# Kernel optimization log

Hardware: AMD Instinct MI355X
Metric: run time of the kernel (lower is better)

Reference implementation:

```python
import jax, jax.numpy as jnp
import numpy as np

D_MODEL = 768
N_HEADS = 12
NUM_EXPERTS = 4
TOP_K = 2
SPAN_LEN = 64
GATE_HIDDEN = 128


def setup_inputs() -> dict:
    key = jax.random.key(0)
    ks = jax.random.split(key, 14)
    B, T, C, E = 4, 4096, D_MODEL, NUM_EXPERTS
    s = 0.02
    return {
        "hidden_states": jax.random.normal(ks[0], (B, T, C), jnp.float32),
        "Wq": jax.random.normal(ks[1], (E, C, C), jnp.float32) * s,
        "bq": jnp.zeros((E, C), jnp.float32),
        "Wk": jax.random.normal(ks[2], (E, C, C), jnp.float32) * s,
        "bk": jnp.zeros((E, C), jnp.float32),
        "Wv": jax.random.normal(ks[3], (E, C, C), jnp.float32) * s,
        "bv": jnp.zeros((E, C), jnp.float32),
        "gW1": jax.random.normal(ks[4], (GATE_HIDDEN, C), jnp.float32) * s,
        "gb1": jnp.zeros((GATE_HIDDEN,), jnp.float32),
        "gW2": jax.random.normal(ks[5], (E, GATE_HIDDEN), jnp.float32) * s,
        "gb2": jnp.zeros((E,), jnp.float32),
        "Wo": jax.random.normal(ks[6], (C, C), jnp.float32) * s,
        "bo": jnp.zeros((C,), jnp.float32),
    }


def _moe_proj(w, x, W, b):
    # per-expert projection then gate-weighted sum over experts
    # x: (B,N,S,C), W: (E,O,C), w: (B,N,E)
    proj = jnp.einsum("bnsc,eoc->ebnso", x, W)          # (E,B,N,S,C)
    out = jnp.einsum("bne,ebnso->bnso", w, proj)
    out = out + jnp.einsum("bne,eo->bno", w, b)[:, :, None, :]
    return out


def reference(hidden_states, Wq, bq, Wk, bk, Wv, bv, gW1, gb1, gW2, gb2, Wo, bo):
    B, T, C = hidden_states.shape
    S, H, E, K = SPAN_LEN, N_HEADS, NUM_EXPERTS, TOP_K
    Dh = C // H
    N = T // S  # T is a multiple of span_len -> no padding, all-ones masks
    x = hidden_states.reshape(B, N, S, C)

    # gating: mean-pool per span -> MLP -> top-k softmax scattered to E slots
    pooled = x.mean(axis=2)                                  # (B,N,C)
    h = jax.nn.relu(pooled @ gW1.T + gb1)
    logits = h @ gW2.T + gb2                                 # (B,N,E)
    vals, idx = jax.lax.top_k(logits, K)
    sm = jax.nn.softmax(vals, axis=-1)                       # (B,N,K)
    w = jnp.sum(jax.nn.one_hot(idx, E, dtype=sm.dtype) * sm[..., None], axis=-2)  # (B,N,E)
    entropy = -jnp.mean(jnp.sum(w * jnp.log(jnp.clip(w, 1e-9)), axis=-1))

    # gate-weighted expert QKV projections
    q = _moe_proj(w, x, Wq, bq).reshape(B, N, S, H, Dh)
    k = _moe_proj(w, x, Wk, bk).reshape(B, N, S, H, Dh)
    v = _moe_proj(w, x, Wv, bv).reshape(B, N, S, H, Dh)

    # per-span attention (mask is all ones; dropout in eval mode)
    scores = jnp.einsum("bnshd,bnthd->bnhst", q, k) / jnp.sqrt(jnp.float32(Dh))
    attn = jax.nn.softmax(scores, axis=-1)
    out = jnp.einsum("bnhst,bnthd->bnshd", attn, v).reshape(B, T, C)
    out = out @ Wo.T + bo
    return out, entropy
```

## Files before the change

### kernel.cpp

```cpp
#include <hip/hip_runtime.h>
#include <hip/hip_bf16.h>
#include <hip/hip_fp16.h>

typedef _Float16 f16;
typedef _Float16 f16x8 __attribute__((ext_vector_type(8)));
typedef _Float16 f16x4 __attribute__((ext_vector_type(4)));
typedef float f32x4 __attribute__((ext_vector_type(4)));

constexpr int B = 4;
constexpr int T = 4096;
constexpr int C = 768;
constexpr int NH = 12;
constexpr int DH = 64;
constexpr int E = 4;
constexpr int SPAN = 64;
constexpr int N = T / SPAN;
constexpr int BN = B * N;
constexpr int GH = 128;
constexpr int BTC = B * T * C;

constexpr int U_X  = BTC / 8;
constexpr int U_WE = E * C * C / 8;
constexpr int U_WO = C * C / 8;
constexpr int U_TOT = U_X + 3 * U_WE + U_WO;

__global__ void cvt_all(const float* __restrict__ x,
                        const float* __restrict__ Wq, const float* __restrict__ Wk,
                        const float* __restrict__ Wv, const float* __restrict__ Wo,
                        f16* __restrict__ x16,
                        f16* __restrict__ Wq16, f16* __restrict__ Wk16,
                        f16* __restrict__ Wv16, f16* __restrict__ Wo16) {
    int i = blockIdx.x * blockDim.x + threadIdx.x;
    int stride = gridDim.x * blockDim.x;
    for (; i < U_TOT; i += stride) {
        const float* src; f16* dst; int u;
        if (i < U_X)                { src = x;  dst = x16;  u = i; }
        else if (i < U_X + U_WE)    { src = Wq; dst = Wq16; u = i - U_X; }
        else if (i < U_X + 2*U_WE)  { src = Wk; dst = Wk16; u = i - U_X - U_WE; }
        else if (i < U_X + 3*U_WE)  { src = Wv; dst = Wv16; u = i - U_X - 2*U_WE; }
        else                        { src = Wo; dst = Wo16; u = i - U_X - 3*U_WE; }
        float4 a = ((const float4*)src)[2 * u];
        float4 b = ((const float4*)src)[2 * u + 1];
        f16x8 o;
        o[0] = (f16)a.x; o[1] = (f16)a.y; o[2] = (f16)a.z; o[3] = (f16)a.w;
        o[4] = (f16)b.x; o[5] = (f16)b.y; o[6] = (f16)b.z; o[7] = (f16)b.w;
        ((f16x8*)dst)[u] = o;
    }
}

__global__ void gate_kernel(const float* __restrict__ x,
                            const float* __restrict__ gW1, const float* __restrict__ gb1,
                            const float* __restrict__ gW2, const float* __restrict__ gb2,
                            int* __restrict__ eidx, float* __restrict__ ewts,
                            float* __restrict__ ent_partial) {
    int span = blockIdx.x;
    int tid = threadIdx.x;
    __shared__ float pooled[C];
    __shared__ float h[GH];
    __shared__ float logits[E];

    const float* xb = x + (size_t)span * SPAN * C;
    for (int c = tid; c < C; c += 256) {
        float s = 0.f;
        #pragma unroll 8
        for (int t = 0; t < SPAN; ++t) s += xb[t * C + c];
        pooled[c] = s * (1.f / 64.f);
    }
    __syncthreads();

    if (tid < GH) {
        float acc = gb1[tid];
        const float* wrow = gW1 + (size_t)tid * C;
        #pragma unroll 8
        for (int c = 0; c < C; ++c) acc += pooled[c] * wrow[c];
        h[tid] = acc > 0.f ? acc : 0.f;
    }
    __syncthreads();

    if (tid < E) {
        float acc = gb2[tid];
        const float* wrow = gW2 + (size_t)tid * GH;
        #pragma unroll 8
        for (int j = 0; j < GH; ++j) acc += h[j] * wrow[j];
        logits[tid] = acc;
    }
    __syncthreads();

    if (tid == 0) {
        int i0 = 0; float v0 = logits[0];
        for (int e = 1; e < E; ++e) { if (logits[e] > v0) { v0 = logits[e]; i0 = e; } }
        int i1 = -1; float v1 = -3.0e38f;
        for (int e = 0; e < E; ++e) { if (e != i0 && logits[e] > v1) { v1 = logits[e]; i1 = e; } }
        float bq_ = expf(v1 - v0);
        float s = 1.f + bq_;
        float sm0 = 1.f / s;
        float sm1 = bq_ / s;
        eidx[span * 2 + 0] = i0;
        eidx[span * 2 + 1] = i1;
        ewts[span * 2 + 0] = sm0;
        ewts[span * 2 + 1] = sm1;
        float p0 = fmaxf(sm0, 1e-9f), p1 = fmaxf(sm1, 1e-9f);
        ent_partial[span] = sm0 * logf(p0) + sm1 * logf(p1);
    }
}

__global__ void entropy_kernel(const float* __restrict__ ent_partial, float* __restrict__ out_ent) {
    __shared__ float sh[256];
    int tid = threadIdx.x;
    sh[tid] = ent_partial[tid];
    __syncthreads();
    for (int s = 128; s > 0; s >>= 1) {
        if (tid < s) sh[tid] += sh[tid + s];
        __syncthreads();
    }
    if (tid == 0) *out_ent = -sh[0] * (1.0f / (float)BN);
}

__global__ __launch_bounds__(256) void qkv_mfma(
    const f16* __restrict__ xh,
    const f16* __restrict__ Wq16, const float* __restrict__ bq,
    const f16* __restrict__ Wk16, const float* __restrict__ bk,
    const f16* __restrict__ Wv16, const float* __restrict__ bv,
    const int* __restrict__ eidx, const float* __restrict__ ewts,
    f16* __restrict__ q16, f16* __restrict__ k16, f16* __restrict__ vt)
{
    int span  = blockIdx.x;
    int otile = blockIdx.y;
    int proj  = blockIdx.z;

    const f16* W; const float* bias; f16* out;
    if (proj == 0)      { W = Wq16; bias = bq; out = q16; }
    else if (proj == 1) { W = Wk16; bias = bk; out = k16; }
    else                { W = Wv16; bias = bv; out = vt; }

    int e0 = eidx[span * 2 + 0], e1 = eidx[span * 2 + 1];
    float w0 = ewts[span * 2 + 0], w1 = ewts[span * 2 + 1];
    f16 w0h = (f16)w0, w1h = (f16)w1;

    __shared__ f16x8 xs_u[64 * 8];
    __shared__ f16x8 ws_u[256 * 8];

    const f16x8* xu  = (const f16x8*)(xh + (size_t)span * 64 * C);
    const f16x8* Wu0 = (const f16x8*)(W + ((size_t)e0 * C + otile * 256) * (size_t)C);
    const f16x8* Wu1 = (const f16x8*)(W + ((size_t)e1 * C + otile * 256) * (size_t)C);

    int tid = threadIdx.x;
    int lane = tid & 63, wv = tid >> 6;
    int lr = lane & 15, lg = lane >> 4;

    int xr0 = tid >> 3, xu0 = tid & 7;
    f32x4 acc[4][4] = {};

    f16x8 xr[2], w0r[8], w1r[8];
    #pragma unroll
    for (int i = 0; i < 2; ++i) {
        int id = tid + i * 256;
        xr[i] = xu[(id >> 3) * 96 + (id & 7)];
    }
    #pragma unroll
    for (int i = 0; i < 8; ++i) {
        int id = tid + i * 256;
        w0r[i] = Wu0[(size_t)(id >> 3) * 96 + (id & 7)];
        w1r[i] = Wu1[(size_t)(id >> 3) * 96 + (id & 7)];
    }

    for (int kc8 = 0; kc8 < 96; kc8 += 8) {
        #pragma unroll
        for (int i = 0; i < 2; ++i) {
            int id = tid + i * 256;
            int r = id >> 3, u = id & 7;
            xs_u[r * 8 + (u ^ (r & 7))] = xr[i];
        }
        #pragma unroll
        for (int i = 0; i < 8; ++i) {
            int id = tid + i * 256;
            int r = id >> 3, u = id & 7;
            ws_u[r * 8 + (u ^ (r & 7))] = w0r[i] * w0h + w1r[i] * w1h;
        }
        __syncthreads();

        if (kc8 < 88) {
            int kn = kc8 + 8;
            #pragma unroll
            for (int i = 0; i < 2; ++i) {
                int id = tid + i * 256;
                xr[i] = xu[(id >> 3) * 96 + kn + (id & 7)];
            }
            #pragma unroll
            for (int i = 0; i < 8; ++i) {
                int id = tid + i * 256;
                w0r[i] = Wu0[(size_t)(id >> 3) * 96 + kn + (id & 7)];
                w1r[i] = Wu1[(size_t)(id >> 3) * 96 + kn + (id & 7)];
            }
        }

        #pragma unroll
        for (int kk = 0; kk < 2; ++kk) {
            int ub = kk * 4 + lg;
            f16x8 afrag[4], bfrag[4];
            #pragma unroll
            for (int m = 0; m < 4; ++m) {
                int r = m * 16 + lr;
                afrag[m] = xs_u[r * 8 + (ub ^ (r & 7))];
            }
            #pragma unroll
            for (int n = 0; n < 4; ++n) {
                int r = wv * 64 + n * 16 + lr;
                bfrag[n] = ws_u[r * 8 + (ub ^ (r & 7))];
            }
            #pragma unroll
            for (int m = 0; m < 4; ++m)
                #pragma unroll
                for (int n = 0; n < 4; ++n)
                    acc[m][n] = __builtin_amdgcn_mfma_f32_16x16x32_f16(afrag[m], bfrag[n], acc[m][n], 0, 0, 0);
        }
        __syncthreads();
    }

    if (proj == 2) {
        f16* vtb = out + (size_t)span * C * 64;
        #pragma unroll
        for (int n = 0; n < 4; ++n) {
            int col = otile * 256 + wv * 64 + n * 16 + lr;
            float be = w0 * bias[(size_t)e0 * C + col] + w1 * bias[(size_t)e1 * C + col];
            #pragma unroll
            for (int m = 0; m < 4; ++m) {
                f16x4 pk;
                #pragma unroll
                for (int r = 0; r < 4; ++r) pk[r] = (f16)(acc[m][n][r] + be);
                *(f16x4*)&vtb[(size_t)col * 64 + m * 16 + lg * 4] = pk;
            }
        }
    } else {
        f16* outb = out + (size_t)span * 64 * C;
        #pragma unroll
        for (int n = 0; n < 4; ++n) {
            int col = otile * 256 + wv * 64 + n * 16 + lr;
            float be = w0 * bias[(size_t)e0 * C + col] + w1 * bias[(size_t)e1 * C + col];
            #pragma unroll
            for (int m = 0; m < 4; ++m) {
                #pragma unroll
                for (int r = 0; r < 4; ++r) {
                    int row = m * 16 + lg * 4 + r;
                    outb[(size_t)row * C + col] = (f16)(acc[m][n][r] + be);
                }
            }
        }
    }
}

__global__ __launch_bounds__(256) void attn_mfma(
    const f16* __restrict__ q16, const f16* __restrict__ k16,
    const f16* __restrict__ vt, f16* __restrict__ a16)
{
    int h = blockIdx.x, span = blockIdx.y;
    __shared__ __align__(16) f16 Klds[64 * 72];
    __shared__ __align__(16) f16 Vlds[64 * 72];
    __shared__ __align__(16) f16 Plds[64 * 72];

    int tid = threadIdx.x;
    int lane = tid & 63, mt = tid >> 6;
    int lr = lane & 15, lg = lane >> 4;

    const f16x8* ku = (const f16x8*)k16;
    const f16x8* vu = (const f16x8*)vt;
    #pragma unroll
    for (int i = 0; i < 2; ++i) {
        int id = tid + i * 256;
        int r = id >> 3, u = id & 7;
        *(f16x8*)&Klds[r * 72 + u * 8] = ku[(size_t)span * 6144 + (size_t)r * 96 + h * 8 + u];
        *(f16x8*)&Vlds[r * 72 + u * 8] = vu[(size_t)span * 6144 + (size_t)(h * 64 + r) * 8 + u];
    }
    __syncthreads();

    const f16x8* qu = (const f16x8*)q16;
    f16x8 qa[2];
    #pragma unroll
    for (int kk = 0; kk < 2; ++kk)
        qa[kk] = qu[(size_t)span * 6144 + (size_t)(mt * 16 + lr) * 96 + h * 8 + kk * 4 + lg];

    f32x4 accs[4] = {};
    #pragma unroll
    for (int nt = 0; nt < 4; ++nt) {
        #pragma unroll
        for (int kk = 0; kk < 2; ++kk) {
            f16x8 kb = *(const f16x8*)&Klds[(nt * 16 + lr) * 72 + kk * 32 + lg * 8];
            accs[nt] = __builtin_amdgcn_mfma_f32_16x16x32_f16(qa[kk], kb, accs[nt], 0, 0, 0);
        }
    }

    #pragma unroll
    for (int nt = 0; nt < 4; ++nt) accs[nt] *= 0.125f;
    f32x4 m4;
    #pragma unroll
    for (int r = 0; r < 4; ++r)
        m4[r] = fmaxf(fmaxf(accs[0][r], accs[1][r]), fmaxf(accs[2][r], accs[3][r]));
    #pragma unroll
    for (int st = 1; st < 16; st <<= 1) {
        #pragma unroll
        for (int r = 0; r < 4; ++r) m4[r] = fmaxf(m4[r], __shfl_xor(m4[r], st));
    }
    f32x4 ps[4];
    f32x4 sum4 = {0.f, 0.f, 0.f, 0.f};
    #pragma unroll
    for (int nt = 0; nt < 4; ++nt)
        #pragma unroll
        for (int r = 0; r < 4; ++r) {
            ps[nt][r] = __expf(accs[nt][r] - m4[r]);
            sum4[r] += ps[nt][r];
        }
    #pragma unroll
    for (int st = 1; st < 16; st <<= 1) {
        #pragma unroll
        for (int r = 0; r < 4; ++r) sum4[r] += __shfl_xor(sum4[r], st);
    }
    f32x4 inv4;
    #pragma unroll
    for (int r = 0; r < 4; ++r) inv4[r] = 1.0f / sum4[r];

    #pragma unroll
    for (int nt = 0; nt < 4; ++nt)
        #pragma unroll
        for (int r = 0; r < 4; ++r)
            Plds[(mt * 16 + lg * 4 + r) * 72 + nt * 16 + lr] = (f16)ps[nt][r];
    __syncthreads();

    f16x8 pa[2];
    #pragma unroll
    for (int kkt = 0; kkt < 2; ++kkt)
        pa[kkt] = *(const f16x8*)&Plds[(mt * 16 + lr) * 72 + kkt * 32 + lg * 8];
    f32x4 acco[4] = {};
    #pragma unroll
    for (int nt = 0; nt < 4; ++nt) {
        #pragma unroll
        for (int kkt = 0; kkt < 2; ++kkt) {
            f16x8 vb = *(const f16x8*)&Vlds[(nt * 16 + lr) * 72 + kkt * 32 + lg * 8];
            acco[nt] = __builtin_amdgcn_mfma_f32_16x16x32_f16(pa[kkt], vb, acco[nt], 0, 0, 0);
        }
    }

    #pragma unroll
    for (int nt = 0; nt < 4; ++nt)
        #pragma unroll
        for (int r = 0; r < 4; ++r)
            Klds[(mt * 16 + lg * 4 + r) * 72 + nt * 16 + lr] = (f16)(acco[nt][r] * inv4[r]);
    __syncthreads();

    int row = mt * 16 + (lane >> 2);
    int u2 = (lane & 3) * 2;
    f16x8 o0 = *(const f16x8*)&Klds[row * 72 + u2 * 8];
    f16x8 o1 = *(const f16x8*)&Klds[row * 72 + u2 * 8 + 8];
    f16x8* au = (f16x8*)a16;
    au[(size_t)span * 6144 + (size_t)row * 96 + h * 8 + u2]     = o0;
    au[(size_t)span * 6144 + (size_t)row * 96 + h * 8 + u2 + 1] = o1;
}

__global__ __launch_bounds__(512) void outproj_mfma(
    const f16* __restrict__ ah, const f16* __restrict__ Wo16,
    const float* __restrict__ bo, float* __restrict__ Y)
{
    int rt = blockIdx.x;
    int otile = blockIdx.y;

    __shared__ f16x8 as_u[128 * 8];
    __shared__ f16x8 ws_u[256 * 8];

    const f16x8* au  = (const f16x8*)(ah + (size_t)rt * 128 * C);
    const f16x8* Wou = (const f16x8*)(Wo16 + (size_t)otile * 256 * C);

    int tid = threadIdx.x;
    int lane = tid & 63, wv = tid >> 6;
    int lr = lane & 15, lg = lane >> 4;
    int wm = (wv >> 2) * 64;
    int wn = (wv & 3) * 64;

    f32x4 acc[4][4] = {};

    for (int kc8 = 0; kc8 < 96; kc8 += 8) {
        #pragma unroll
        for (int i = 0; i < 2; ++i) {
            int id = tid + i * 512;
            int r = id >> 3, u = id & 7;
            as_u[r * 8 + (u ^ (r & 7))] = au[(size_t)r * 96 + kc8 + u];
        }
        #pragma unroll
        for (int i = 0; i < 4; ++i) {
            int id = tid + i * 512;
            int r = id >> 3, u = id & 7;
            ws_u[r * 8 + (u ^ (r & 7))] = Wou[(size_t)r * 96 + kc8 + u];
        }
        __syncthreads();
        #pragma unroll
        for (int kk = 0; kk < 2; ++kk) {
            int ub = kk * 4 + lg;
            f16x8 afrag[4], bfrag[4];
            #pragma unroll
            for (int m = 0; m < 4; ++m) {
                int r = wm + m * 16 + lr;
                afrag[m] = as_u[r * 8 + (ub ^ (r & 7))];
            }
            #pragma unroll
            for (int n = 0; n < 4; ++n) {
                int r = wn + n * 16 + lr;
                bfrag[n] = ws_u[r * 8 + (ub ^ (r & 7))];
            }
            #pragma unroll
            for (int m = 0; m < 4; ++m)
                #pragma unroll
                for (int n = 0; n < 4; ++n)
                    acc[m][n] = __builtin_amdgcn_mfma_f32_16x16x32_f16(afrag[m], bfrag[n], acc[m][n], 0, 0, 0);
        }
        __syncthreads();
    }

    #pragma unroll
    for (int n = 0; n < 4; ++n) {
        int col = otile * 256 + wn + n * 16 + lr;
        float be = bo[col];
        #pragma unroll
        for (int m = 0; m < 4; ++m) {
            #pragma unroll
            for (int r = 0; r < 4; ++r) {
                int row = rt * 128 + wm + m * 16 + lg * 4 + r;
                Y[(size_t)row * C + col] = acc[m][n][r] + be;
            }
        }
    }
}

extern "C" void kernel_launch(void* const* d_in, const int* in_sizes, int n_in,
                              void* d_out, int out_size, void* d_ws, size_t ws_size,
                              hipStream_t stream) {
    const float* x   = (const float*)d_in[0];
    const float* Wq  = (const float*)d_in[1];
    const float* bq  = (const float*)d_in[2];
    const float* Wk  = (const float*)d_in[3];
    const float* bk  = (const float*)d_in[4];
    const float* Wv  = (const float*)d_in[5];
    const float* bv  = (const float*)d_in[6];
    const float* gW1 = (const float*)d_in[7];
    const float* gb1 = (const float*)d_in[8];
    const float* gW2 = (const float*)d_in[9];
    const float* gb2 = (const float*)d_in[10];
    const float* Wo  = (const float*)d_in[11];
    const float* bo  = (const float*)d_in[12];

    float* out = (float*)d_out;

    char* ws = (char*)d_ws;
    const size_t h_btc = (size_t)BTC * sizeof(f16);
    f16* x16  = (f16*)(ws);
    f16* q16  = (f16*)(ws + 1 * h_btc);
    f16* k16  = (f16*)(ws + 2 * h_btc);
    f16* vt16 = (f16*)(ws + 3 * h_btc);
    f16* a16  = (f16*)(ws + 4 * h_btc);
    size_t off = 5 * h_btc;
    const size_t wsz = (size_t)E * C * C * sizeof(f16);
    f16* Wq16 = (f16*)(ws + off); off += wsz;
    f16* Wk16 = (f16*)(ws + off); off += wsz;
    f16* Wv16 = (f16*)(ws + off); off += wsz;
    f16* Wo16 = (f16*)(ws + off); off += (size_t)C * C * sizeof(f16);
    int*   eidx = (int*)(ws + off); off += 2048;
    float* ewts = (float*)(ws + off); off += 2048;
    float* entp = (float*)(ws + off);

    cvt_all<<<dim3(2048), dim3(256), 0, stream>>>(x, Wq, Wk, Wv, Wo,
                                                  x16, Wq16, Wk16, Wv16, Wo16);

    gate_kernel<<<dim3(BN), dim3(256), 0, stream>>>(x, gW1, gb1, gW2, gb2, eidx, ewts, entp);
    entropy_kernel<<<dim3(1), dim3(256), 0, stream>>>(entp, out + BTC);

    qkv_mfma<<<dim3(BN, 3, 3), dim3(256), 0, stream>>>(x16, Wq16, bq, Wk16, bk, Wv16, bv,
                                                       eidx, ewts, q16, k16, vt16);
    attn_mfma<<<dim3(NH, BN), dim3(256), 0, stream>>>(q16, k16, vt16, a16);
    outproj_mfma<<<dim3(128, 3), dim3(512), 0, stream>>>(a16, Wo16, bo, out);
}
```

Baseline: 219.4 us.

## Double-buffer QKV projection with async global-to-LDS loads and expert mixing in fragments

Replaces the register-staged global loads in the QKV GEMM with direct global_load_lds copies into a double-buffered LDS ring of 32-wide K chunks. Both expert weight tiles are now stored raw in LDS and mixed by gate weight when MFMA fragments are read, rather than before the LDS store. The aim is to overlap memory traffic with MFMA work and cut register pressure, with manual waitcnt, barriers and priority hints. In exchange it uses more LDS (both expert tiles, two buffers), adds a barrier pair per smaller chunk, and repeats the mixing arithmetic in every wave.

```diff
diff --git a/kernel.cpp b/kernel.cpp
--- a/kernel.cpp
+++ b/kernel.cpp
@@ -116,6 +116,19 @@
     if (tid == 0) *out_ent = -sh[0] * (1.0f / (float)BN);
 }
 
+constexpr int QKV_KC    = 32;
+constexpr int QKV_NCH   = C / QKV_KC;
+constexpr int QKV_XU    = 64 * (QKV_KC / 8);
+constexpr int QKV_WU    = 256 * (QKV_KC / 8);
+constexpr int QKV_BUFU  = QKV_XU + 2 * QKV_WU;
+
+__device__ __forceinline__ void async_copy16(const void* g, void* l) {
+    __builtin_amdgcn_global_load_lds(
+        (const __attribute__((address_space(1))) unsigned int*)g,
+        (__attribute__((address_space(3))) unsigned int*)l,
+        16, 0, 0);
+}
+
 __global__ __launch_bounds__(256) void qkv_mfma(
     const f16* __restrict__ xh,
     const f16* __restrict__ Wq16, const float* __restrict__ bq,
@@ -137,8 +150,7 @@
     float w0 = ewts[span * 2 + 0], w1 = ewts[span * 2 + 1];
     f16 w0h = (f16)w0, w1h = (f16)w1;
 
-    __shared__ f16x8 xs_u[64 * 8];
-    __shared__ f16x8 ws_u[256 * 8];
+    __shared__ f16x8 lds_u[2 * QKV_BUFU];
 
     const f16x8* xu  = (const f16x8*)(xh + (size_t)span * 64 * C);
     const f16x8* Wu0 = (const f16x8*)(W + ((size_t)e0 * C + otile * 256) * (size_t)C);
@@ -148,73 +160,79 @@
     int lane = tid & 63, wv = tid >> 6;
     int lr = lane & 15, lg = lane >> 4;
 
-    int xr0 = tid >> 3, xu0 = tid & 7;
+    const f16x8* srcp[9];
+    #pragma unroll
+    for (int j = 0; j < 9; ++j) {
+        int gidx = wv * 576 + j * 64 + lane;
+        const f16x8* base; int t;
+        if (gidx < QKV_XU)                 { base = xu;  t = gidx; }
+        else if (gidx < QKV_XU + QKV_WU)   { base = Wu0; t = gidx - QKV_XU; }
+        else                               { base = Wu1; t = gidx - QKV_XU - QKV_WU; }
+        int g  = t >> 3, p = t & 7;
+        int lw = p ^ (g & 7);
+        int r  = (g << 1) | (lw >> 2);
+        int lu = lw & 3;
+        srcp[j] = base + (size_t)r * 96 + lu;
+    }
+
+    int pA[4], pB[4];
+    #pragma unroll
+    for (int m = 0; m < 4; ++m) {
+        int r = m * 16 + lr;
+        int g = r >> 1, w = ((r & 1) << 2) | lg;
+        pA[m] = (g << 3) | (w ^ (g & 7));
+    }
+    #pragma unroll
+    for (int n = 0; n < 4; ++n) {
+        int r = wv * 64 + n * 16 + lr;
+        int g = r >> 1, w = ((r & 1) << 2) | lg;
+        pB[n] = (g << 3) | (w ^ (g & 7));
+    }
+
     f32x4 acc[4][4] = {};
 
-    f16x8 xr[2], w0r[8], w1r[8];
-    #pragma unroll
-    for (int i = 0; i < 2; ++i) {
-        int id = tid + i * 256;
-        xr[i] = xu[(id >> 3) * 96 + (id & 7)];
-    }
-    #pragma unroll
-    for (int i = 0; i < 8; ++i) {
-        int id = tid + i * 256;
-        w0r[i] = Wu0[(size_t)(id >> 3) * 96 + (id & 7)];
-        w1r[i] = Wu1[(size_t)(id >> 3) * 96 + (id & 7)];
-    }
-
-    for (int kc8 = 0; kc8 < 96; kc8 += 8) {
-        #pragma unroll
-        for (int i = 0; i < 2; ++i) {
-            int id = tid + i * 256;
-            int r = id >> 3, u = id & 7;
-            xs_u[r * 8 + (u ^ (r & 7))] = xr[i];
-        }
-        #pragma unroll
-        for (int i = 0; i < 8; ++i) {
-            int id = tid + i * 256;
-            int r = id >> 3, u = id & 7;
-            ws_u[r * 8 + (u ^ (r & 7))] = w0r[i] * w0h + w1r[i] * w1h;
-        }
-        __syncthreads();
-
-        if (kc8 < 88) {
-            int kn = kc8 + 8;
-            #pragma unroll
-            for (int i = 0; i < 2; ++i) {
-                int id = tid + i * 256;
-                xr[i] = xu[(id >> 3) * 96 + kn + (id & 7)];
-            }
-            #pragma unroll
-            for (int i = 0; i < 8; ++i) {
-                int id = tid + i * 256;
-                w0r[i] = Wu0[(size_t)(id >> 3) * 96 + kn + (id & 7)];
-                w1r[i] = Wu1[(size_t)(id >> 3) * 96 + kn + (id & 7)];
-            }
-        }
-
-        #pragma unroll
-        for (int kk = 0; kk < 2; ++kk) {
-            int ub = kk * 4 + lg;
-            f16x8 afrag[4], bfrag[4];
-            #pragma unroll
-            for (int m = 0; m < 4; ++m) {
-                int r = m * 16 + lr;
-                afrag[m] = xs_u[r * 8 + (ub ^ (r & 7))];
-            }
-            #pragma unroll
-            for (int n = 0; n < 4; ++n) {
-                int r = wv * 64 + n * 16 + lr;
-                bfrag[n] = ws_u[r * 8 + (ub ^ (r & 7))];
-            }
-            #pragma unroll
-            for (int m = 0; m < 4; ++m)
-                #pragma unroll
-                for (int n = 0; n < 4; ++n)
-                    acc[m][n] = __builtin_amdgcn_mfma_f32_16x16x32_f16(afrag[m], bfrag[n], acc[m][n], 0, 0, 0);
-        }
-        __syncthreads();
+    #pragma unroll
+    for (int j = 0; j < 9; ++j) {
+        async_copy16(srcp[j], &lds_u[wv * 576 + j * 64]);
+        srcp[j] += 4;
+    }
+
+    for (int ch = 0; ch < QKV_NCH; ++ch) {
+        if (ch < QKV_NCH - 1) {
+            #pragma unroll
+            for (int j = 0; j < 9; ++j) {
+                async_copy16(srcp[j],
+                             &lds_u[((ch + 1) & 1) * QKV_BUFU + wv * 576 + j * 64]);
+                srcp[j] += 4;
+            }
+            asm volatile("s_waitcnt vmcnt(9)" ::: "memory");
+        } else {
+            asm volatile("s_waitcnt vmcnt(0)" ::: "memory");
+        }
+        __builtin_amdgcn_s_barrier();
+        __builtin_amdgcn_sched_barrier(0);
+
+        const f16x8* Lx = &lds_u[(ch & 1) * QKV_BUFU];
+        const f16x8* L0 = Lx + QKV_XU;
+        const f16x8* L1 = Lx + QKV_XU + QKV_WU;
+
+        f16x8 afrag[4], bfrag[4];
+        #pragma unroll
+        for (int m = 0; m < 4; ++m) afrag[m] = Lx[pA[m]];
+        #pragma unroll
+        for (int n = 0; n < 4; ++n) bfrag[n] = L0[pB[n]] * w0h + L1[pB[n]] * w1h;
+
+        __builtin_amdgcn_s_setprio(1);
+        #pragma unroll
+        for (int m = 0; m < 4; ++m)
+            #pragma unroll
+            for (int n = 0; n < 4; ++n)
+                acc[m][n] = __builtin_amdgcn_mfma_f32_16x16x32_f16(afrag[m], bfrag[n], acc[m][n], 0, 0, 0);
+        __builtin_amdgcn_s_setprio(0);
+
+        asm volatile("" ::: "memory");
+        __builtin_amdgcn_s_barrier();
+        __builtin_amdgcn_sched_barrier(0);
     }
 
     if (proj == 2) {
```

Measured after the change: 265.3 us. 1.21x slower.

## Restructure QKV kernel: full-span X in LDS, direct-register weight fragments

Applied to the files above, without the earlier changes.

The QKV projection now runs one 768-thread block per (span, projection) covering all 768 output columns, instead of three 256-column tiles. The whole 64x768 span of X is loaded once into swizzled LDS, and each wave streams its gate-mixed weight fragments straight from global memory into registers, with no LDS staging and no per-iteration barriers. This removes the repeated X loads across output tiles and the sync overhead. In exchange, weight reads are strided per lane with no software prefetch, and the larger block with 96KB of LDS lowers occupancy.

```diff
diff --git a/kernel.cpp b/kernel.cpp
--- a/kernel.cpp
+++ b/kernel.cpp
@@ -116,7 +116,7 @@
     if (tid == 0) *out_ent = -sh[0] * (1.0f / (float)BN);
 }
 
-__global__ __launch_bounds__(256) void qkv_mfma(
+__global__ __launch_bounds__(768) void qkv_mfma(
     const f16* __restrict__ xh,
     const f16* __restrict__ Wq16, const float* __restrict__ bq,
     const f16* __restrict__ Wk16, const float* __restrict__ bk,
@@ -124,9 +124,8 @@
     const int* __restrict__ eidx, const float* __restrict__ ewts,
     f16* __restrict__ q16, f16* __restrict__ k16, f16* __restrict__ vt)
 {
-    int span  = blockIdx.x;
-    int otile = blockIdx.y;
-    int proj  = blockIdx.z;
+    int span = blockIdx.x;
+    int proj = blockIdx.y;
 
     const f16* W; const float* bias; f16* out;
     if (proj == 0)      { W = Wq16; bias = bq; out = q16; }
@@ -137,111 +136,96 @@
     float w0 = ewts[span * 2 + 0], w1 = ewts[span * 2 + 1];
     f16 w0h = (f16)w0, w1h = (f16)w1;
 
-    __shared__ f16x8 xs_u[64 * 8];
-    __shared__ f16x8 ws_u[256 * 8];
-
-    const f16x8* xu  = (const f16x8*)(xh + (size_t)span * 64 * C);
-    const f16x8* Wu0 = (const f16x8*)(W + ((size_t)e0 * C + otile * 256) * (size_t)C);
-    const f16x8* Wu1 = (const f16x8*)(W + ((size_t)e1 * C + otile * 256) * (size_t)C);
+    __shared__ f16x8 xs[6144];
 
     int tid = threadIdx.x;
+
+    {
+        const f16x8* xu = (const f16x8*)(xh + (size_t)span * 64 * C);
+        int trow = tid / 96;
+        int trem = tid % 96;
+        int grp  = trem & ~7, sub = trem & 7;
+        #pragma unroll
+        for (int j = 0; j < 8; ++j) {
+            int row = j * 8 + trow;
+            xs[row * 96 + grp + (sub ^ (row & 7))] = xu[(size_t)row * 96 + trem];
+        }
+    }
+    __syncthreads();
+
     int lane = tid & 63, wv = tid >> 6;
     int lr = lane & 15, lg = lane >> 4;
-
-    int xr0 = tid >> 3, xu0 = tid & 7;
-    f32x4 acc[4][4] = {};
-
-    f16x8 xr[2], w0r[8], w1r[8];
-    #pragma unroll
-    for (int i = 0; i < 2; ++i) {
-        int id = tid + i * 256;
-        xr[i] = xu[(id >> 3) * 96 + (id & 7)];
-    }
-    #pragma unroll
-    for (int i = 0; i < 8; ++i) {
-        int id = tid + i * 256;
-        w0r[i] = Wu0[(size_t)(id >> 3) * 96 + (id & 7)];
-        w1r[i] = Wu1[(size_t)(id >> 3) * 96 + (id & 7)];
-    }
-
-    for (int kc8 = 0; kc8 < 96; kc8 += 8) {
-        #pragma unroll
-        for (int i = 0; i < 2; ++i) {
-            int id = tid + i * 256;
-            int r = id >> 3, u = id & 7;
-            xs_u[r * 8 + (u ^ (r & 7))] = xr[i];
-        }
-        #pragma unroll
-        for (int i = 0; i < 8; ++i) {
-            int id = tid + i * 256;
-            int r = id >> 3, u = id & 7;
-            ws_u[r * 8 + (u ^ (r & 7))] = w0r[i] * w0h + w1r[i] * w1h;
-        }
-        __syncthreads();
-
-        if (kc8 < 88) {
-            int kn = kc8 + 8;
-            #pragma unroll
-            for (int i = 0; i < 2; ++i) {
-                int id = tid + i * 256;
-                xr[i] = xu[(id >> 3) * 96 + kn + (id & 7)];
-            }
-            #pragma unroll
-            for (int i = 0; i < 8; ++i) {
-                int id = tid + i * 256;
-                w0r[i] = Wu0[(size_t)(id >> 3) * 96 + kn + (id & 7)];
-                w1r[i] = Wu1[(size_t)(id >> 3) * 96 + kn + (id & 7)];
-            }
-        }
-
-        #pragma unroll
-        for (int kk = 0; kk < 2; ++kk) {
-            int ub = kk * 4 + lg;
-            f16x8 afrag[4], bfrag[4];
-            #pragma unroll
-            for (int m = 0; m < 4; ++m) {
-                int r = m * 16 + lr;
-                afrag[m] = xs_u[r * 8 + (ub ^ (r & 7))];
-            }
+    int wm = wv & 1;
+    int wn = wv >> 1;
+
+    const f16x8* Wu0 = (const f16x8*)(W + (size_t)e0 * C * C);
+    const f16x8* Wu1 = (const f16x8*)(W + (size_t)e1 * C * C);
+
+    size_t wrow_base[8];
+    #pragma unroll
+    for (int n = 0; n < 8; ++n)
+        wrow_base[n] = (size_t)(wn * 128 + n * 16 + lr) * 96 + lg;
+
+    int arow[2];
+    #pragma unroll
+    for (int m = 0; m < 2; ++m) arow[m] = wm * 32 + m * 16 + lr;
+
+    f32x4 acc[2][8] = {};
+
+    for (int it = 0; it < 24; ++it) {
+        f16x8 af[2];
+        {
+            int grp = (it >> 1) * 8;
+            int s4  = (it & 1) * 4 + lg;
+            #pragma unroll
+            for (int m = 0; m < 2; ++m)
+                af[m] = xs[arow[m] * 96 + grp + (s4 ^ (arow[m] & 7))];
+        }
+        #pragma unroll
+        for (int h = 0; h < 2; ++h) {
+            f16x8 b0r[4], b1r[4];
             #pragma unroll
             for (int n = 0; n < 4; ++n) {
-                int r = wv * 64 + n * 16 + lr;
-                bfrag[n] = ws_u[r * 8 + (ub ^ (r & 7))];
-            }
-            #pragma unroll
-            for (int m = 0; m < 4; ++m)
+                size_t uidx = wrow_base[h * 4 + n] + (size_t)it * 4;
+                b0r[n] = Wu0[uidx];
+                b1r[n] = Wu1[uidx];
+            }
+            #pragma unroll
+            for (int n = 0; n < 4; ++n) {
+                f16x8 bf = b0r[n] * w0h + b1r[n] * w1h;
                 #pragma unroll
-                for (int n = 0; n < 4; ++n)
-                    acc[m][n] = __builtin_amdgcn_mfma_f32_16x16x32_f16(afrag[m], bfrag[n], acc[m][n], 0, 0, 0);
-        }
-        __syncthreads();
+                for (int m = 0; m < 2; ++m)
+                    acc[m][h * 4 + n] =
+                        __builtin_amdgcn_mfma_f32_16x16x32_f16(af[m], bf, acc[m][h * 4 + n], 0, 0, 0);
+            }
+        }
     }
 
     if (proj == 2) {
         f16* vtb = out + (size_t)span * C * 64;
         #pragma unroll
-        for (int n = 0; n < 4; ++n) {
-            int col = otile * 256 + wv * 64 + n * 16 + lr;
+        for (int n = 0; n < 8; ++n) {
+            int col = wn * 128 + n * 16 + lr;
             float be = w0 * bias[(size_t)e0 * C + col] + w1 * bias[(size_t)e1 * C + col];
             #pragma unroll
-            for (int m = 0; m < 4; ++m) {
+            for (int m = 0; m < 2; ++m) {
                 f16x4 pk;
                 #pragma unroll
                 for (int r = 0; r < 4; ++r) pk[r] = (f16)(acc[m][n][r] + be);
-                *(f16x4*)&vtb[(size_t)col * 64 + m * 16 + lg * 4] = pk;
+                *(f16x4*)&vtb[(size_t)col * 64 + wm * 32 + m * 16 + lg * 4] = pk;
             }
         }
     } else {
         f16* outb = out + (size_t)span * 64 * C;
         #pragma unroll
-        for (int n = 0; n < 4; ++n) {
-            int col = otile * 256 + wv * 64 + n * 16 + lr;
+        for (int n = 0; n < 8; ++n) {
+            int col = wn * 128 + n * 16 + lr;
             float be = w0 * bias[(size_t)e0 * C + col] + w1 * bias[(size_t)e1 * C + col];
             #pragma unroll
-            for (int m = 0; m < 4; ++m) {
+            for (int m = 0; m < 2; ++m) {
                 #pragma unroll
                 for (int r = 0; r < 4; ++r) {
-                    int row = m * 16 + lg * 4 + r;
+                    int row = wm * 32 + m * 16 + lg * 4 + r;
                     outb[(size_t)row * C + col] = (f16)(acc[m][n][r] + be);
                 }
             }
@@ -470,8 +454,8 @@
     gate_kernel<<<dim3(BN), dim3(256), 0, stream>>>(x, gW1, gb1, gW2, gb2, eidx, ewts, entp);
     entropy_kernel<<<dim3(1), dim3(256), 0, stream>>>(entp, out + BTC);
 
-    qkv_mfma<<<dim3(BN, 3, 3), dim3(256), 0, stream>>>(x16, Wq16, bq, Wk16, bk, Wv16, bv,
-                                                       eidx, ewts, q16, k16, vt16);
+    qkv_mfma<<<dim3(BN, 3), dim3(768), 0, stream>>>(x16, Wq16, bq, Wk16, bk, Wv16, bv,
+                                                    eidx, ewts, q16, k16, vt16);
     attn_mfma<<<dim3(NH, BN), dim3(256), 0, stream>>>(q16, k16, vt16, a16);
     outproj_mfma<<<dim3(128, 3), dim3(512), 0, stream>>>(a16, Wo16, bo, out);
 }
```

Result: slower. 508.6 us (+131.9%).
